# Kernel optimization log

Measured on AMD Instinct MI355X. Metric: run time of the kernel, lower is better.

Reference implementation:

```python
import jax, jax.numpy as jnp
import numpy as np

N_CUST, N_PROD, D, H, OUT, E = 100000, 10000, 128, 128, 64, 500000
RELS = ["purchase", "redeem", "transfer_to", "transfer_from", "dividend_from"]


def setup_inputs() -> dict:
    key = jax.random.key(0)
    ks = jax.random.split(key, 40)
    inp = {}
    inp["x_cust"] = jax.random.normal(ks[0], (N_CUST, D), jnp.float32)
    inp["x_prod"] = jax.random.normal(ks[1], (N_PROD, D), jnp.float32)
    for i, r in enumerate(RELS):
        inp["src_" + r] = jax.random.randint(ks[2 + 2 * i], (E,), 0, N_CUST)
        inp["dst_" + r] = jax.random.randint(ks[3 + 2 * i], (E,), 0, N_PROD)
    s = 0.05
    names = [("W_gcn", (D, H)), ("b_gcn", (H,)), ("Ws_gat", (D, H)), ("Wd_gat", (D, H)),
             ("a_s_gat", (H,)), ("a_d_gat", (H,)), ("b_gat", (H,)),
             ("Wl_to", (D, H)), ("b_to", (H,)), ("Wr_to", (D, H)),
             ("Wl_from", (D, H)), ("b_from", (H,)), ("Wr_from", (D, H)),
             ("Wl_div", (D, H)), ("b_div", (H,)), ("Wr_div", (D, H)),
             ("W_out", (H, OUT)), ("b_out", (OUT,))]
    for i, (n, shp) in enumerate(names):
        inp[n] = jax.random.normal(ks[12 + i], shp, jnp.float32) * s
    return inp


def _gcn(x_src, src, dst, W, b):
    # symmetric-norm bipartite GCN: transform then gather->scale->scatter
    deg_s = jax.ops.segment_sum(jnp.ones_like(src, jnp.float32), src, N_CUST)
    deg_d = jax.ops.segment_sum(jnp.ones_like(dst, jnp.float32), dst, N_PROD)
    norm = jax.lax.rsqrt(deg_s[src] * deg_d[dst])  # [E]
    h = x_src @ W  # [N_CUST, H]
    return jax.ops.segment_sum(norm[:, None] * h[src], dst, N_PROD) + b


def _gat(x_src, x_dst, src, dst, Ws, Wd, a_s, a_d, b):
    # single-head bipartite GAT with edge-softmax over incoming edges at dst
    hs = x_src @ Ws                     # [N_CUST, H]
    ls = hs @ a_s                       # [N_CUST]
    ld = (x_dst @ Wd) @ a_d             # [N_PROD]
    logit = jax.nn.leaky_relu(ls[src] + ld[dst], 0.2)  # [E]
    m = jax.ops.segment_max(logit, dst, N_PROD)
    e = jnp.exp(logit - m[dst])
    den = jax.ops.segment_sum(e, dst, N_PROD)
    alpha = e / den[dst]
    return jax.ops.segment_sum(alpha[:, None] * hs[src], dst, N_PROD) + b


def _sage(x_src, x_dst, src, dst, Wl, bl, Wr):
    # mean-aggregate raw src features, then linear; plus root transform of dst
    s = jax.ops.segment_sum(x_src[src], dst, N_PROD)
    c = jax.ops.segment_sum(jnp.ones_like(dst, jnp.float32), dst, N_PROD)
    mean = s / jnp.maximum(c, 1.0)[:, None]
    return mean @ Wl + bl + x_dst @ Wr


def reference(x_cust, x_prod, src_purchase, dst_purchase, src_redeem, dst_redeem,
              src_transfer_to, dst_transfer_to, src_transfer_from, dst_transfer_from,
              src_dividend_from, dst_dividend_from,
              W_gcn, b_gcn, Ws_gat, Wd_gat, a_s_gat, a_d_gat, b_gat,
              Wl_to, b_to, Wr_to, Wl_from, b_from, Wr_from, Wl_div, b_div, Wr_div,
              W_out, b_out):
    prod = _gcn(x_cust, src_purchase, dst_purchase, W_gcn, b_gcn)
    prod = prod + _gat(x_cust, x_prod, src_redeem, dst_redeem, Ws_gat, Wd_gat, a_s_gat, a_d_gat, b_gat)
    prod = prod + _sage(x_cust, x_prod, src_transfer_to, dst_transfer_to, Wl_to, b_to, Wr_to)
    prod = prod + _sage(x_cust, x_prod, src_transfer_from, dst_transfer_from, Wl_from, b_from, Wr_from)
    prod = prod + _sage(x_cust, x_prod, src_dividend_from, dst_dividend_from, Wl_div, b_div, Wr_div)
    prod = jax.nn.relu(prod)  # HeteroConv(aggr='sum') then relu
    return prod @ W_out + b_out  # [N_PROD, OUT]
```

## Files before the change

### kernel.cpp

```cpp
#include <hip/hip_runtime.h>

#define WF 64
#define CAP 128
#define CH 2048
#define LC 32
#define NGMAX 160
#define BINCAP 3584

typedef int v4i __attribute__((ext_vector_type(4)));
typedef short short8 __attribute__((ext_vector_type(8)));
typedef float f32x4 __attribute__((ext_vector_type(4)));
typedef float f32x2 __attribute__((ext_vector_type(2)));

#if __has_builtin(__builtin_amdgcn_cvt_f32_fp8) && __has_builtin(__builtin_amdgcn_cvt_pk_fp8_f32)
#define HW_FP8 1
#endif

__device__ __forceinline__ void gload_lds16(const void* g, void* lds) {
    __builtin_amdgcn_global_load_lds(
        (const __attribute__((address_space(1))) unsigned int*)g,
        (__attribute__((address_space(3))) unsigned int*)lds, 16, 0, 0);
}

__device__ __forceinline__ unsigned fp8enc1(float x) {
    unsigned b = __builtin_bit_cast(unsigned, x);
    unsigned s = (b >> 24) & 0x80u;
    int E = (b >> 23) & 0xff;
    unsigned m = b & 0x7fffffu;
    unsigned mr = (m + 0x7ffffu + ((m >> 20) & 1u)) >> 20;
    int e8 = E - 120 + (int)(mr >> 3);
    mr &= 7u;
    if (e8 <= 0) return s;
    if (e8 > 15) { e8 = 15; mr = 7u; }
    return s | ((unsigned)e8 << 3) | mr;
}
__device__ __forceinline__ float fp8dec1(unsigned u8) {
    unsigned f = ((u8 & 0x80u) << 24) | (((u8 & 0x7fu) << 20) + 0x3C000000u);
    return (u8 & 0x7fu) ? __builtin_bit_cast(float, f) : 0.f;
}
__device__ __forceinline__ unsigned fp8pack4(float4 u) {
#ifdef HW_FP8
    int r = __builtin_amdgcn_cvt_pk_fp8_f32(u.x, u.y, 0, false);
    r = __builtin_amdgcn_cvt_pk_fp8_f32(u.z, u.w, r, true);
    return (unsigned)r;
#else
    return fp8enc1(u.x) | (fp8enc1(u.y) << 8) | (fp8enc1(u.z) << 16) | (fp8enc1(u.w) << 24);
#endif
}
__device__ __forceinline__ void accP2(float w, unsigned u, f32x2& A, f32x2& B) {
    f32x2 w2 = {w, w};
#if defined(HW_FP8) && __has_builtin(__builtin_amdgcn_cvt_pk_f32_fp8)
    f32x2 d0 = __builtin_amdgcn_cvt_pk_f32_fp8((int)u, false);
    f32x2 d1 = __builtin_amdgcn_cvt_pk_f32_fp8((int)u, true);
    A = __builtin_elementwise_fma(w2, d0, A);
    B = __builtin_elementwise_fma(w2, d1, B);
#elif defined(HW_FP8)
    f32x2 d0 = {__builtin_amdgcn_cvt_f32_fp8((int)u, 0), __builtin_amdgcn_cvt_f32_fp8((int)u, 1)};
    f32x2 d1 = {__builtin_amdgcn_cvt_f32_fp8((int)u, 2), __builtin_amdgcn_cvt_f32_fp8((int)u, 3)};
    A = __builtin_elementwise_fma(w2, d0, A);
    B = __builtin_elementwise_fma(w2, d1, B);
#else
    A[0] = fmaf(w, fp8dec1(u & 0xffu), A[0]);
    A[1] = fmaf(w, fp8dec1((u >> 8) & 0xffu), A[1]);
    B[0] = fmaf(w, fp8dec1((u >> 16) & 0xffu), B[0]);
    B[1] = fmaf(w, fp8dec1(u >> 24), B[1]);
#endif
}

__device__ __forceinline__ short bf16r(float x) {
    unsigned u = __builtin_bit_cast(unsigned, x);
    u += 0x7fffu + ((u >> 16) & 1u);
    return (short)(u >> 16);
}
__device__ __forceinline__ void bfsplit(float x, short& hi, short& lo) {
    unsigned u = __builtin_bit_cast(unsigned, x);
    hi = (short)(u >> 16);
    float fh = __builtin_bit_cast(float, u & 0xffff0000u);
    lo = bf16r(x - fh);
}

__global__ void k_init(int* deg_s, int nc2, int* bincur, int nb, int ZB,
                       const float* __restrict__ Ws, const float* __restrict__ Wd,
                       const float* __restrict__ as_, const float* __restrict__ ad_,
                       const float* __restrict__ bg, const float* __restrict__ bga,
                       const float* __restrict__ bto, const float* __restrict__ bfr,
                       const float* __restrict__ bdv,
                       const float* __restrict__ Wg, const float* __restrict__ Wlt,
                       const float* __restrict__ Wlf, const float* __restrict__ Wld,
                       const float* __restrict__ Wrt, const float* __restrict__ Wrf,
                       const float* __restrict__ Wrd, const float* __restrict__ Wo,
                       float* vs, float* vd, float* bsum,
                       short* wth, short* wtl, short* woth, short* wotl) {
    int b = blockIdx.x, t = threadIdx.x;
    if (b < ZB) {
        int i = b * 256 + t;
        if (i < nc2) deg_s[i] = 0;
        if (i < nb) bincur[i] = 0;
    } else if (b == ZB) {
        if (t < 128) {
            float a = 0.f, bb = 0.f;
            for (int h = 0; h < 128; ++h) {
                a += Ws[t * 128 + h] * as_[h];
                bb += Wd[t * 128 + h] * ad_[h];
            }
            vs[t] = a; vd[t] = bb;
            bsum[t] = bg[t] + bga[t] + bto[t] + bfr[t] + bdv[t];
        }
    } else if (b < ZB + 385) {
        int e = (b - ZB - 1) * 256 + t;
        int h = e / 768;
        int q = e - h * 768;
        int m = q >> 7, k = q & 127;
        int src = k * 128 + h;
        float val;
        switch (m) {
            case 0: val = Wg[src]; break;
            case 1: val = Ws[src]; break;
            case 2: val = Wlt[src]; break;
            case 3: val = Wlf[src]; break;
            case 4: val = Wld[src]; break;
            default: val = Wrt[src] + Wrf[src] + Wrd[src]; break;
        }
        short hi, lo;
        bfsplit(val, hi, lo);
        int kswz = k ^ ((h & 7) << 3);
        int idx = h * 768 + m * 128 + kswz;
        wth[idx] = hi; wtl[idx] = lo;
    } else {
        int e = (b - ZB - 385) * 256 + t;
        int o = e >> 7, k = e & 127;
        short hi, lo;
        bfsplit(Wo[k * 64 + o], hi, lo);
        woth[e] = hi; wotl[e] = lo;
    }
}

__global__ __launch_bounds__(256) void k_bin(
    const int* s0, const int* s1, const int* s2, const int* s3, const int* s4,
    const int* d0, const int* d1, const int* d2, const int* d3, const int* d4,
    int* bincur, int* gbin, int* deg_s, int E, int NP, int ng,
    int bpjE, int B0, int HB4, int CB,
    const float* __restrict__ xc, const float* __restrict__ xp,
    const float* __restrict__ vs, const float* __restrict__ vd,
    unsigned* __restrict__ xh, float* __restrict__ lsb, float* __restrict__ ldb,
    short* __restrict__ xph, short* __restrict__ xpl, int NC) {
    __shared__ int lcnt[NGMAX];
    __shared__ int lbase[NGMAX];
    __shared__ int lbin[NGMAX * LC];
    int b = blockIdx.x, t = threadIdx.x;
    if (b < B0) {
        int rel = b / bpjE;
        int blk = b - rel * bpjE;
        const int *sp, *dp;
        switch (rel) {
            case 0: sp = s0; dp = d0; break;
            case 1: sp = s1; dp = d1; break;
            case 2: sp = s2; dp = d2; break;
            case 3: sp = s3; dp = d3; break;
            default: sp = s4; dp = d4; break;
        }
        for (int i = t; i < ng; i += 256) lcnt[i] = 0;
        __syncthreads();
        int* bc = bincur + rel * ng;
        int* gb0 = gbin + (size_t)rel * ng * BINCAP;
        int start = blk * CH;
        int q0 = start + t * 8;
#pragma unroll
        for (int c = 0; c < 8; c += 4) {
            int q = q0 + c;
            if (q >= E) break;
            if (q + 3 < E) {
                v4i dv = __builtin_nontemporal_load((const v4i*)(dp + q));
                v4i sv = __builtin_nontemporal_load((const v4i*)(sp + q));
                int dd[4] = {dv.x, dv.y, dv.z, dv.w};
                int ss[4] = {sv.x, sv.y, sv.z, sv.w};
#pragma unroll
                for (int z = 0; z < 4; ++z) {
                    int bin = dd[z] >> 6;
                    int pk = (ss[z] << 6) | (dd[z] & 63);
                    int pos = atomicAdd(&lcnt[bin], 1);
                    if (pos < LC) lbin[bin * LC + pos] = pk;
                    else {
                        int g = atomicAdd(bc + bin, 1);
                        if (g < BINCAP) gb0[(size_t)bin * BINCAP + g] = pk;
                    }
                }
            } else {
                for (int i = q; i < E; ++i) {
                    int d = dp[i];
                    int bin = d >> 6;
                    int pk = (sp[i] << 6) | (d & 63);
                    int pos = atomicAdd(&lcnt[bin], 1);
                    if (pos < LC) lbin[bin * LC + pos] = pk;
                    else {
                        int g = atomicAdd(bc + bin, 1);
                        if (g < BINCAP) gb0[(size_t)bin * BINCAP + g] = pk;
                    }
                }
            }
        }
        __syncthreads();
        if (t < ng) {
            int c = min(lcnt[t], LC);
            lbase[t] = atomicAdd(bc + t, c);
        }
        __syncthreads();
        int wv = t >> 6, lane = t & 63;
        for (int bin = wv; bin < ng; bin += 4) {
            int c = min(lcnt[bin], LC);
            int gbase = lbase[bin];
            int* gp = gb0 + (size_t)bin * BINCAP;
            for (int i = lane; i < c; i += 64) {
                int g = gbase + i;
                if (g < BINCAP) gp[g] = lbin[bin * LC + i];
            }
        }
    } else if (b < B0 + HB4) {
        int q = ((b - B0) * 256 + t) * 4;
        if (q >= E) return;
        if (q + 3 < E) {
            v4i v = __builtin_nontemporal_load((const v4i*)(s0 + q));
            atomicAdd(deg_s + v.x, 1); atomicAdd(deg_s + v.y, 1);
            atomicAdd(deg_s + v.z, 1); atomicAdd(deg_s + v.w, 1);
        } else {
            for (int i = q; i < E; ++i) atomicAdd(deg_s + s0[i], 1);
        }
    } else if (b < B0 + HB4 + CB) {
        int row = (b - B0 - HB4) * 8 + (t >> 5);
        int q = t & 31;
        if (row >= NC) return;
        float4 u = *(const float4*)(xc + (size_t)row * 128 + 4 * q);
        float4 v = *(const float4*)(vs + 4 * q);
        float s = u.x * v.x + u.y * v.y + u.z * v.z + u.w * v.w;
        xh[(size_t)row * 32 + q] = fp8pack4(u);
#pragma unroll
        for (int o = 16; o; o >>= 1) s += __shfl_xor(s, o, WF);
        if (q == 0) lsb[row] = s;
    } else {
        int row = (b - B0 - HB4 - CB) * 4 + (t >> 6);
        int l = t & 63;
        if (row >= NP) return;
        const float* xr = xp + (size_t)row * 128;
        float x0 = xr[2 * l], x1 = xr[2 * l + 1];
        short h0, lo0, h1, lo1;
        bfsplit(x0, h0, lo0);
        bfsplit(x1, h1, lo1);
        ((unsigned*)(xph + (size_t)row * 128))[l] =
            (unsigned)(unsigned short)h0 | ((unsigned)(unsigned short)h1 << 16);
        ((unsigned*)(xpl + (size_t)row * 128))[l] =
            (unsigned)(unsigned short)lo0 | ((unsigned)(unsigned short)lo1 << 16);
        float s = x0 * vd[2 * l] + x1 * vd[2 * l + 1];
        for (int o = 32; o; o >>= 1) s += __shfl_down(s, o, WF);
        if (l == 0) ldb[row] = s;
    }
}

__global__ __launch_bounds__(256) void k_aggf(
    const int* __restrict__ gbin, const int* __restrict__ bincur,
    const int* __restrict__ deg_s,
    const float* __restrict__ ls, const float* __restrict__ ld,
    const unsigned* __restrict__ xh,
    short* __restrict__ aggH, short* __restrict__ aggL,
    int NP, int ng) {
    __shared__ int cnt[16];
    __shared__ int buck[16][CAP + 4];
    __shared__ float wbuf[4][CAP + 4];
    int t = threadIdx.x;
    int rel = blockIdx.x / (4 * ng);
    int rem = blockIdx.x - rel * 4 * ng;
    int grp = rem >> 2, sub = rem & 3;
    if (t < 16) cnt[t] = 0;
    __syncthreads();
    int binid = rel * ng + grp;
    int n = min(bincur[binid], BINCAP);
    const int* bsrc = gbin + (size_t)binid * BINCAP;
    for (int i = t; i < n; i += 256) {
        int e = bsrc[i];
        int lp = e & 63;
        if ((lp >> 4) == sub) {
            int li = lp & 15;
            int pos = atomicAdd(&cnt[li], 1);
            if (pos < CAP) buck[li][pos] = e >> 6;
        }
    }
    __syncthreads();
    if (t < 16) {
        int c = min(cnt[t], CAP);
        buck[t][c] = 0; buck[t][c + 1] = 0; buck[t][c + 2] = 0;
    }
    __syncthreads();

    int wv = t >> 6, l = t & 63;
    int g = l >> 4, q8 = l & 15;

    for (int r = 0; r < 4; ++r) {
        int li = r * 4 + wv;
        int p = grp * 64 + sub * 16 + li;
        bool valid = (p < NP);
        int m = valid ? min(cnt[li], CAP) : 0;

        if (rel == 0) {
            float rd = rsqrtf((float)m);
            for (int e = l; e < m; e += WF)
                wbuf[wv][e] = rsqrtf((float)deg_s[buck[li][e]]) * rd;
        } else if (rel == 1) {
            if (m > 0) {
                float ldp = ld[p];
                float ml = -3.4e38f, dl = 0.f;
                for (int e = l; e < m; e += WF) {
                    float tt = ls[buck[li][e]] + ldp;
                    tt = tt > 0.f ? tt : 0.2f * tt;
                    wbuf[wv][e] = tt;
                    if (tt > ml) { dl = dl * __expf(ml - tt) + 1.f; ml = tt; }
                    else dl += __expf(tt - ml);
                }
                for (int o = 32; o; o >>= 1) {
                    float m2 = __shfl_xor(ml, o, WF), d2 = __shfl_xor(dl, o, WF);
                    float mm = fmaxf(ml, m2);
                    dl = dl * __expf(ml - mm) + d2 * __expf(m2 - mm);
                    ml = mm;
                }
                float inv = 1.f / dl;
                for (int e = l; e < m; e += WF)
                    wbuf[wv][e] = __expf(wbuf[wv][e] - ml) * inv;
            }
        } else {
            float sc = 1.f / fmaxf((float)m, 1.f);
            for (int e = l; e < m; e += WF) wbuf[wv][e] = sc;
        }
        if (l == 0) { wbuf[wv][m] = 0.f; wbuf[wv][m + 1] = 0.f; wbuf[wv][m + 2] = 0.f; }
        __builtin_amdgcn_wave_barrier();

        f32x2 a0 = {0.f, 0.f}, a1 = {0.f, 0.f}, a2 = {0.f, 0.f}, a3 = {0.f, 0.f};
        int nq = (m + 3) >> 2;
        int j = 0;
        for (; j + 4 <= nq; j += 4) {
            int ss[4]; float wk[4]; uint2 uu[4];
#pragma unroll
            for (int z = 0; z < 4; ++z) {
                int e = 4 * (j + z) + g;
                ss[z] = buck[li][e];
                wk[z] = wbuf[wv][e];
            }
#pragma unroll
            for (int z = 0; z < 4; ++z)
                uu[z] = *(const uint2*)(xh + (size_t)ss[z] * 32 + 2 * q8);
#pragma unroll
            for (int z = 0; z < 4; ++z) {
                accP2(wk[z], uu[z].x, a0, a1);
                accP2(wk[z], uu[z].y, a2, a3);
            }
        }
        for (; j < nq; ++j) {
            int e = 4 * j + g;
            int s0 = buck[li][e];
            float w0 = wbuf[wv][e];
            uint2 u0 = *(const uint2*)(xh + (size_t)s0 * 32 + 2 * q8);
            accP2(w0, u0.x, a0, a1);
            accP2(w0, u0.y, a2, a3);
        }

#pragma unroll
        for (int o = 16; o <= 32; o <<= 1) {
            a0[0] += __shfl_xor(a0[0], o, WF); a0[1] += __shfl_xor(a0[1], o, WF);
            a1[0] += __shfl_xor(a1[0], o, WF); a1[1] += __shfl_xor(a1[1], o, WF);
            a2[0] += __shfl_xor(a2[0], o, WF); a2[1] += __shfl_xor(a2[1], o, WF);
            a3[0] += __shfl_xor(a3[0], o, WF); a3[1] += __shfl_xor(a3[1], o, WF);
        }

        if (valid && l < 16) {
            short8 hv, lv;
            short hh, ll;
            bfsplit(a0[0], hh, ll); hv[0] = hh; lv[0] = ll;
            bfsplit(a0[1], hh, ll); hv[1] = hh; lv[1] = ll;
            bfsplit(a1[0], hh, ll); hv[2] = hh; lv[2] = ll;
            bfsplit(a1[1], hh, ll); hv[3] = hh; lv[3] = ll;
            bfsplit(a2[0], hh, ll); hv[4] = hh; lv[4] = ll;
            bfsplit(a2[1], hh, ll); hv[5] = hh; lv[5] = ll;
            bfsplit(a3[0], hh, ll); hv[6] = hh; lv[6] = ll;
            bfsplit(a3[1], hh, ll); hv[7] = hh; lv[7] = ll;
            size_t base = ((size_t)rel * NP + p) * 128 + 8 * q8;
            *(short8*)(aggH + base) = hv;
            *(short8*)(aggL + base) = lv;
        }
    }
}

__global__ __launch_bounds__(256, 2) void k_gemm_out(
    const short* __restrict__ aggH, const short* __restrict__ aggL,
    const short* __restrict__ wth, const short* __restrict__ wtl,
    const short* __restrict__ woth, const short* __restrict__ wotl,
    const float* __restrict__ bsum, const float* __restrict__ bout,
    float* __restrict__ out, int NP) {
    __shared__ short bsh[128 * 128];
    __shared__ short bsl[128 * 128];
    __shared__ short c1h[16][136];
    __shared__ short c1l[16][136];
    int t = threadIdx.x;
    int w = t >> 6, l = t & 63;
    int lr = l & 15, lq = l >> 4;
    int kq = lq * 8;
    int row0 = blockIdx.x * 16;
    int ar = row0 + lr;
    if (ar > NP - 1) ar = NP - 1;

    int srow = w * 4;
    int lbyte = 0;
    (void)lbyte;

    f32x4 acc[2] = {};

#pragma unroll
    for (int m = 0; m < 6; ++m) {
        __syncthreads();
        {
            const char* srch = (const char*)wth + m * 256;
            const char* srcl = (const char*)wtl + m * 256;
            int hb = srow + (l >> 4);
            int cb = (l & 15) * 16;
#pragma unroll
            for (int i = 0; i < 8; ++i) {
                int h = i * 16 + hb;
                gload_lds16(srch + h * 1536 + cb, (char*)bsh + (i * 16 + srow) * 256);
            }
#pragma unroll
            for (int i = 0; i < 8; ++i) {
                int h = i * 16 + hb;
                gload_lds16(srcl + h * 1536 + cb, (char*)bsl + (i * 16 + srow) * 256);
            }
        }
        __syncthreads();

        const short* ahp = aggH + ((size_t)m * NP + ar) * 128;
        const short* alp = aggL + ((size_t)m * NP + ar) * 128;
#pragma unroll
        for (int kk = 0; kk < 4; ++kk) {
            int ko = kk * 32 + kq;
            short8 ah = *(const short8*)(ahp + ko);
            short8 al = *(const short8*)(alp + ko);
#pragma unroll
            for (int ci = 0; ci < 2; ++ci) {
                int hcol = 32 * w + 16 * ci + lr;
                int boff = hcol * 256 + ((ko * 2) ^ ((hcol & 7) << 4));
                short8 bh = *(const short8*)((const char*)bsh + boff);
                short8 bl = *(const short8*)((const char*)bsl + boff);
                acc[ci] = __builtin_amdgcn_mfma_f32_16x16x32_bf16(ah, bh, acc[ci], 0, 0, 0);
                acc[ci] = __builtin_amdgcn_mfma_f32_16x16x32_bf16(al, bh, acc[ci], 0, 0, 0);
                acc[ci] = __builtin_amdgcn_mfma_f32_16x16x32_bf16(ah, bl, acc[ci], 0, 0, 0);
            }
        }
    }

#pragma unroll
    for (int ci = 0; ci < 2; ++ci) {
        int col = 32 * w + 16 * ci + lr;
        float bs = bsum[col];
#pragma unroll
        for (int r = 0; r < 4; ++r) {
            float v = acc[ci][r] + bs;
            v = v > 0.f ? v : 0.f;
            short hh, ll;
            bfsplit(v, hh, ll);
            int rl = 4 * lq + r;
            c1h[rl][col] = hh;
            c1l[rl][col] = ll;
        }
    }
    __syncthreads();

    f32x4 acc2 = {};
#pragma unroll
    for (int kb = 0; kb < 4; ++kb) {
        int kof = kb * 32 + kq;
        short8 a2h = *(const short8*)&c1h[lr][kof];
        short8 a2l = *(const short8*)&c1l[lr][kof];
        int o = 16 * w + lr;
        short8 b2h = *(const short8*)(woth + o * 128 + kof);
        short8 b2l = *(const short8*)(wotl + o * 128 + kof);
        acc2 = __builtin_amdgcn_mfma_f32_16x16x32_bf16(a2h, b2h, acc2, 0, 0, 0);
        acc2 = __builtin_amdgcn_mfma_f32_16x16x32_bf16(a2l, b2h, acc2, 0, 0, 0);
        acc2 = __builtin_amdgcn_mfma_f32_16x16x32_bf16(a2h, b2l, acc2, 0, 0, 0);
    }
    int col = 16 * w + lr;
    float bo = bout[col];
#pragma unroll
    for (int r = 0; r < 4; ++r) {
        int row = row0 + 4 * lq + r;
        if (row < NP) out[(size_t)row * 64 + col] = acc2[r] + bo;
    }
}

extern "C" void kernel_launch(void* const* d_in, const int* in_sizes, int n_in,
                              void* d_out, int out_size, void* d_ws, size_t ws_size,
                              hipStream_t stream) {
    const float* x_cust = (const float*)d_in[0];
    const float* x_prod = (const float*)d_in[1];
    const int* src_pur = (const int*)d_in[2];  const int* dst_pur = (const int*)d_in[3];
    const int* src_red = (const int*)d_in[4];  const int* dst_red = (const int*)d_in[5];
    const int* src_to  = (const int*)d_in[6];  const int* dst_to  = (const int*)d_in[7];
    const int* src_fr  = (const int*)d_in[8];  const int* dst_fr  = (const int*)d_in[9];
    const int* src_dv  = (const int*)d_in[10]; const int* dst_dv  = (const int*)d_in[11];
    const float* W_gcn = (const float*)d_in[12];
    const float* b_gcn = (const float*)d_in[13];
    const float* Ws_gat = (const float*)d_in[14]; const float* Wd_gat = (const float*)d_in[15];
    const float* a_s = (const float*)d_in[16]; const float* a_d = (const float*)d_in[17];
    const float* b_gat = (const float*)d_in[18];
    const float* Wl_to = (const float*)d_in[19]; const float* b_to = (const float*)d_in[20];
    const float* Wr_to = (const float*)d_in[21];
    const float* Wl_fr = (const float*)d_in[22]; const float* b_fr = (const float*)d_in[23];
    const float* Wr_fr = (const float*)d_in[24];
    const float* Wl_dv = (const float*)d_in[25]; const float* b_dv = (const float*)d_in[26];
    const float* Wr_dv = (const float*)d_in[27];
    const float* W_out = (const float*)d_in[28]; const float* b_out = (const float*)d_in[29];
    float* out = (float*)d_out;

    int NC = in_sizes[0] / 128;
    int NP = in_sizes[1] / 128;
    int E  = in_sizes[2];
    int ng = (NP + 63) >> 6;

    char* ws = (char*)d_ws;
    size_t off = 0;
    auto alloc = [&](size_t bytes) -> void* {
        void* p = ws + off;
        off = (off + bytes + 255) & ~(size_t)255;
        return p;
    };
    int*      deg_s  = (int*)alloc((size_t)NC * 4);
    int*      bincur = (int*)alloc((size_t)5 * NGMAX * 4);
    int*      gbin   = (int*)alloc((size_t)5 * NGMAX * BINCAP * 4);
    float*    lsb    = (float*)alloc((size_t)NC * 4);
    float*    ldb    = (float*)alloc((size_t)NP * 4);
    float*    vs     = (float*)alloc(512);
    float*    vd     = (float*)alloc(512);
    float*    bsum   = (float*)alloc(512);
    short*    wth    = (short*)alloc((size_t)98304 * 2);
    short*    wtl    = (short*)alloc((size_t)98304 * 2);
    short*    woth   = (short*)alloc((size_t)8192 * 2);
    short*    wotl   = (short*)alloc((size_t)8192 * 2);
    unsigned* xh     = (unsigned*)alloc((size_t)NC * 32 * 4);
    short*    aggH   = (short*)alloc((size_t)6 * NP * 128 * 2);
    short*    aggL   = (short*)alloc((size_t)6 * NP * 128 * 2);
    short*    xph    = aggH + (size_t)5 * NP * 128;
    short*    xpl    = aggL + (size_t)5 * NP * 128;

    int ZB = (NC + 255) / 256;
    k_init<<<ZB + 1 + 384 + 32, 256, 0, stream>>>(deg_s, NC, bincur, 5 * ng, ZB,
                                                  Ws_gat, Wd_gat, a_s, a_d,
                                                  b_gcn, b_gat, b_to, b_fr, b_dv,
                                                  W_gcn, Wl_to, Wl_fr, Wl_dv,
                                                  Wr_to, Wr_fr, Wr_dv, W_out,
                                                  vs, vd, bsum, wth, wtl, woth, wotl);

    int bpjE = (E + CH - 1) / CH;
    int bpj4 = ((E + 3) / 4 + 255) / 256;
    int B0 = 5 * bpjE, HB4 = bpj4, CB = (NC + 7) / 8, PB = (NP + 3) / 4;
    k_bin<<<B0 + HB4 + CB + PB, 256, 0, stream>>>(
        src_pur, src_red, src_to, src_fr, src_dv,
        dst_pur, dst_red, dst_to, dst_fr, dst_dv,
        bincur, gbin, deg_s, E, NP, ng, bpjE, B0, HB4, CB,
        x_cust, x_prod, vs, vd, xh, lsb, ldb, xph, xpl, NC);

    k_aggf<<<5 * ng * 4, 256, 0, stream>>>(gbin, bincur, deg_s, lsb, ldb, xh,
                                           aggH, aggL, NP, ng);

    k_gemm_out<<<(NP + 15) / 16, 256, 0, stream>>>(
        aggH, aggL, wth, wtl, woth, wotl, bsum, b_out, out, NP);
}
```

Baseline: 280.9 us.

## Prefetch gathered source rows into LDS via async global_load_lds before weight computation

```diff
diff --git a/kernel.cpp b/kernel.cpp
--- a/kernel.cpp
+++ b/kernel.cpp
@@ -263,8 +263,9 @@
     short* __restrict__ aggH, short* __restrict__ aggL,
     int NP, int ng) {
     __shared__ int cnt[16];
-    __shared__ int buck[16][CAP + 4];
+    __shared__ int buck[16][CAP + 8];
     __shared__ float wbuf[4][CAP + 4];
+    __shared__ int stg[4][4096];
     int t = threadIdx.x;
     int rel = blockIdx.x / (4 * ng);
     int rem = blockIdx.x - rel * 4 * ng;
@@ -286,18 +287,31 @@
     __syncthreads();
     if (t < 16) {
         int c = min(cnt[t], CAP);
-        buck[t][c] = 0; buck[t][c + 1] = 0; buck[t][c + 2] = 0;
+#pragma unroll
+        for (int z = 0; z < 7; ++z) buck[t][c + z] = 0;
     }
     __syncthreads();
 
     int wv = t >> 6, l = t & 63;
     int g = l >> 4, q8 = l & 15;
+    int sub8 = l >> 3, ch = l & 7;
+    char* sb = (char*)stg[wv];
 
     for (int r = 0; r < 4; ++r) {
         int li = r * 4 + wv;
         int p = grp * 64 + sub * 16 + li;
         bool valid = (p < NP);
         int m = valid ? min(cnt[li], CAP) : 0;
+        int nst = (m + 7) >> 3;
+
+#pragma unroll
+        for (int i = 0; i < 16; ++i) {
+            if (i < nst) {
+                int es = 8 * i + sub8;
+                int srow = buck[li][es];
+                gload_lds16((const char*)xh + (size_t)srow * 128 + ch * 16, sb + i * 1024);
+            }
+        }
 
         if (rel == 0) {
             float rd = rsqrtf((float)m);
@@ -331,31 +345,16 @@
         if (l == 0) { wbuf[wv][m] = 0.f; wbuf[wv][m + 1] = 0.f; wbuf[wv][m + 2] = 0.f; }
         __builtin_amdgcn_wave_barrier();
 
+        asm volatile("s_waitcnt vmcnt(0)" ::: "memory");
+        __builtin_amdgcn_sched_barrier(0);
+
         f32x2 a0 = {0.f, 0.f}, a1 = {0.f, 0.f}, a2 = {0.f, 0.f}, a3 = {0.f, 0.f};
         int nq = (m + 3) >> 2;
-        int j = 0;
-        for (; j + 4 <= nq; j += 4) {
-            int ss[4]; float wk[4]; uint2 uu[4];
-#pragma unroll
-            for (int z = 0; z < 4; ++z) {
-                int e = 4 * (j + z) + g;
-                ss[z] = buck[li][e];
-                wk[z] = wbuf[wv][e];
-            }
-#pragma unroll
-            for (int z = 0; z < 4; ++z)
-                uu[z] = *(const uint2*)(xh + (size_t)ss[z] * 32 + 2 * q8);
-#pragma unroll
-            for (int z = 0; z < 4; ++z) {
-                accP2(wk[z], uu[z].x, a0, a1);
-                accP2(wk[z], uu[z].y, a2, a3);
-            }
-        }
-        for (; j < nq; ++j) {
+#pragma unroll 4
+        for (int j = 0; j < nq; ++j) {
             int e = 4 * j + g;
-            int s0 = buck[li][e];
             float w0 = wbuf[wv][e];
-            uint2 u0 = *(const uint2*)(xh + (size_t)s0 * 32 + 2 * q8);
+            uint2 u0 = *(const uint2*)(sb + e * 128 + q8 * 8);
             accP2(w0, u0.x, a0, a1);
             accP2(w0, u0.y, a2, a3);
         }
@@ -405,8 +404,6 @@
     if (ar > NP - 1) ar = NP - 1;
 
     int srow = w * 4;
-    int lbyte = 0;
-    (void)lbyte;
 
     f32x4 acc[2] = {};
 
```

After: 321.2 us. +14.3%, slower.

## Process 32 rows per block in output GEMM to reuse staged weights

Applied to the files above, without the earlier changes.

```diff
diff --git a/kernel.cpp b/kernel.cpp
--- a/kernel.cpp
+++ b/kernel.cpp
@@ -392,23 +392,25 @@
     const short* __restrict__ woth, const short* __restrict__ wotl,
     const float* __restrict__ bsum, const float* __restrict__ bout,
     float* __restrict__ out, int NP) {
-    __shared__ short bsh[128 * 128];
-    __shared__ short bsl[128 * 128];
-    __shared__ short c1h[16][136];
-    __shared__ short c1l[16][136];
+    __shared__ char smem[65536];
+    short* bsh = (short*)smem;
+    short* bsl = (short*)(smem + 32768);
+    short (*c1h)[136] = (short(*)[136])smem;
+    short (*c1l)[136] = (short(*)[136])(smem + 32768);
     int t = threadIdx.x;
     int w = t >> 6, l = t & 63;
     int lr = l & 15, lq = l >> 4;
     int kq = lq * 8;
-    int row0 = blockIdx.x * 16;
-    int ar = row0 + lr;
-    if (ar > NP - 1) ar = NP - 1;
+    int row0 = blockIdx.x * 32;
+    int ar[2];
+#pragma unroll
+    for (int hh = 0; hh < 2; ++hh) {
+        int a = row0 + 16 * hh + lr;
+        ar[hh] = a > NP - 1 ? NP - 1 : a;
+    }
 
     int srow = w * 4;
-    int lbyte = 0;
-    (void)lbyte;
-
-    f32x4 acc[2] = {};
+    f32x4 acc[2][2] = {};
 
 #pragma unroll
     for (int m = 0; m < 6; ++m) {
@@ -431,62 +433,74 @@
         }
         __syncthreads();
 
-        const short* ahp = aggH + ((size_t)m * NP + ar) * 128;
-        const short* alp = aggL + ((size_t)m * NP + ar) * 128;
-#pragma unroll
-        for (int kk = 0; kk < 4; ++kk) {
-            int ko = kk * 32 + kq;
-            short8 ah = *(const short8*)(ahp + ko);
-            short8 al = *(const short8*)(alp + ko);
-#pragma unroll
-            for (int ci = 0; ci < 2; ++ci) {
-                int hcol = 32 * w + 16 * ci + lr;
-                int boff = hcol * 256 + ((ko * 2) ^ ((hcol & 7) << 4));
-                short8 bh = *(const short8*)((const char*)bsh + boff);
-                short8 bl = *(const short8*)((const char*)bsl + boff);
-                acc[ci] = __builtin_amdgcn_mfma_f32_16x16x32_bf16(ah, bh, acc[ci], 0, 0, 0);
-                acc[ci] = __builtin_amdgcn_mfma_f32_16x16x32_bf16(al, bh, acc[ci], 0, 0, 0);
-                acc[ci] = __builtin_amdgcn_mfma_f32_16x16x32_bf16(ah, bl, acc[ci], 0, 0, 0);
-            }
-        }
-    }
-
+#pragma unroll
+        for (int hh = 0; hh < 2; ++hh) {
+            const short* ahp = aggH + ((size_t)m * NP + ar[hh]) * 128;
+            const short* alp = aggL + ((size_t)m * NP + ar[hh]) * 128;
+#pragma unroll
+            for (int kk = 0; kk < 4; ++kk) {
+                int ko = kk * 32 + kq;
+                short8 ah = *(const short8*)(ahp + ko);
+                short8 al = *(const short8*)(alp + ko);
+#pragma unroll
+                for (int ci = 0; ci < 2; ++ci) {
+                    int hcol = 32 * w + 16 * ci + lr;
+                    int boff = hcol * 256 + ((ko * 2) ^ ((hcol & 7) << 4));
+                    short8 bh = *(const short8*)((const char*)bsh + boff);
+                    short8 bl = *(const short8*)((const char*)bsl + boff);
+                    acc[hh][ci] = __builtin_amdgcn_mfma_f32_16x16x32_bf16(ah, bh, acc[hh][ci], 0, 0, 0);
+                    acc[hh][ci] = __builtin_amdgcn_mfma_f32_16x16x32_bf16(al, bh, acc[hh][ci], 0, 0, 0);
+                    acc[hh][ci] = __builtin_amdgcn_mfma_f32_16x16x32_bf16(ah, bl, acc[hh][ci], 0, 0, 0);
+                }
+            }
+        }
+    }
+
+    __syncthreads();
+
+#pragma unroll
+    for (int hh = 0; hh < 2; ++hh)
 #pragma unroll
     for (int ci = 0; ci < 2; ++ci) {
         int col = 32 * w + 16 * ci + lr;
         float bs = bsum[col];
 #pragma unroll
         for (int r = 0; r < 4; ++r) {
-            float v = acc[ci][r] + bs;
+            float v = acc[hh][ci][r] + bs;
             v = v > 0.f ? v : 0.f;
-            short hh, ll;
-            bfsplit(v, hh, ll);
-            int rl = 4 * lq + r;
-            c1h[rl][col] = hh;
-            c1l[rl][col] = ll;
+            short hi2, lo2;
+            bfsplit(v, hi2, lo2);
+            int rl = 16 * hh + 4 * lq + r;
+            c1h[rl][col] = hi2;
+            c1l[rl][col] = lo2;
         }
     }
     __syncthreads();
 
-    f32x4 acc2 = {};
+    f32x4 acc2[2] = {};
 #pragma unroll
     for (int kb = 0; kb < 4; ++kb) {
         int kof = kb * 32 + kq;
-        short8 a2h = *(const short8*)&c1h[lr][kof];
-        short8 a2l = *(const short8*)&c1l[lr][kof];
         int o = 16 * w + lr;
         short8 b2h = *(const short8*)(woth + o * 128 + kof);
         short8 b2l = *(const short8*)(wotl + o * 128 + kof);
-        acc2 = __builtin_amdgcn_mfma_f32_16x16x32_bf16(a2h, b2h, acc2, 0, 0, 0);
-        acc2 = __builtin_amdgcn_mfma_f32_16x16x32_bf16(a2l, b2h, acc2, 0, 0, 0);
-        acc2 = __builtin_amdgcn_mfma_f32_16x16x32_bf16(a2h, b2l, acc2, 0, 0, 0);
+#pragma unroll
+        for (int hh = 0; hh < 2; ++hh) {
+            short8 a2h = *(const short8*)&c1h[16 * hh + lr][kof];
+            short8 a2l = *(const short8*)&c1l[16 * hh + lr][kof];
+            acc2[hh] = __builtin_amdgcn_mfma_f32_16x16x32_bf16(a2h, b2h, acc2[hh], 0, 0, 0);
+            acc2[hh] = __builtin_amdgcn_mfma_f32_16x16x32_bf16(a2l, b2h, acc2[hh], 0, 0, 0);
+            acc2[hh] = __builtin_amdgcn_mfma_f32_16x16x32_bf16(a2h, b2l, acc2[hh], 0, 0, 0);
+        }
     }
     int col = 16 * w + lr;
     float bo = bout[col];
 #pragma unroll
+    for (int hh = 0; hh < 2; ++hh)
+#pragma unroll
     for (int r = 0; r < 4; ++r) {
-        int row = row0 + 4 * lq + r;
-        if (row < NP) out[(size_t)row * 64 + col] = acc2[r] + bo;
+        int row = row0 + 16 * hh + 4 * lq + r;
+        if (row < NP) out[(size_t)row * 64 + col] = acc2[hh][r] + bo;
     }
 }
 
@@ -564,6 +578,6 @@
     k_aggf<<<5 * ng * 4, 256, 0, stream>>>(gbin, bincur, deg_s, lsb, ldb, xh,
                                            aggH, aggL, NP, ng);
 
-    k_gemm_out<<<(NP + 15) / 16, 256, 0, stream>>>(
+    k_gemm_out<<<(NP + 31) / 32, 256, 0, stream>>>(
         aggH, aggL, wth, wtl, woth, wotl, bsum, b_out, out, NP);
 }
```

Result: no change. 278.3 us (-0.9%).
